# Kernel tuning notes

Measured on AMD Instinct MI355X. Metric: run time of the kernel, lower is better.

## Reference

```python
import jax, jax.numpy as jnp
import numpy as np


def setup_inputs() -> dict:
    key = jax.random.key(0)
    ks = jax.random.split(key, 4)
    B, C, H, W = 4, 512, 64, 64
    A = 512  # attention_dim
    x = jax.random.normal(ks[0], (B, C, H, W), dtype=jnp.float32)
    # 1x1 conv weights as [out_ch, in_ch] matrices (kaiming-like scale)
    scale = np.sqrt(2.0 / C).astype(np.float32)
    Wq = jax.random.normal(ks[1], (A, C), dtype=jnp.float32) * scale
    Wk = jax.random.normal(ks[2], (A, C), dtype=jnp.float32) * scale
    Wv = jax.random.normal(ks[3], (C, C), dtype=jnp.float32) * scale
    bq = jnp.zeros((A,), dtype=jnp.float32)
    bk = jnp.zeros((A,), dtype=jnp.float32)
    bv = jnp.zeros((C,), dtype=jnp.float32)
    return {"x": x, "Wq": Wq, "bq": bq, "Wk": Wk, "bk": bk, "Wv": Wv, "bv": bv}


def reference(x, Wq, bq, Wk, bk, Wv, bv):
    B, C, H, W = x.shape
    N = H * W
    xf = x.reshape(B, C, N)  # [B, C, N]
    # 1x1 convs == per-pixel channel matmuls
    q = jnp.einsum('ac,bcn->bna', Wq, xf) + bq[None, None, :]   # [B, N, A] (query, permuted)
    k = jnp.einsum('ac,bcn->ban', Wk, xf) + bk[None, :, None]   # [B, A, N] (key)
    v = jnp.einsum('oc,bcn->bno', Wv, xf) + bv[None, None, :]   # [B, N, C] (value, permuted)
    attn = jnp.einsum('bna,bam->bnm', q, k)                     # [B, N, N]
    attn = jax.nn.softmax(attn, axis=-2)                        # softmax over dim=-2 (queries)
    out = jnp.einsum('bnm,bmc->bnc', attn, v)                   # [B, N, C]
    # Faithful to torch: .view(B, C, H, W) reinterprets the [B, N, C] buffer
    out = out.reshape(B, C, H, W)
    return x + 0.1 * out
```

## Files before the change

kernel.cpp:

```cpp
#include <hip/hip_runtime.h>
#include <stdint.h>


#define LDT 40
#define SUB 5120

typedef _Float16 f16x8 __attribute__((ext_vector_type(8)));
typedef float f32x4 __attribute__((ext_vector_type(4)));

template <int ASRC, int EPI>
__global__ void __launch_bounds__(256, 2) gemm_f16(
    const _Float16* __restrict__ Ap, long lda, long zsa,
    const _Float16* __restrict__ Bp, long ldb, long zsb,
    int kslice,
    const _Float16* __restrict__ fs16, long zsl,
    float* __restrict__ outF, _Float16* __restrict__ outH, long ldc, long zso,
    const float* __restrict__ bias0, const float* __restrict__ bias1,
    const float* __restrict__ xadd,
    float* __restrict__ pmax, float* __restrict__ psum, long zsp,
    float alpha)
{
  __shared__ _Float16 smem[4 * SUB];
  _Float16* sA0 = smem;
  _Float16* sA1 = smem + SUB;
  _Float16* sB0 = smem + 2 * SUB;
  _Float16* sB1 = smem + 3 * SUB;

  const int z = blockIdx.z;
  const long i0 = (long)blockIdx.x * 128;
  const long j0 = (long)blockIdx.y * 128;
  const int t = (int)threadIdx.x;
  const int lane = t & 63;
  const int wv = t >> 6;
  const int quad = lane >> 4;
  const int lrow = lane & 15;
  const int wm = (wv & 1) << 6;
  const int wn = (wv >> 1) << 6;

  const int r0 = t >> 2;
  const int s0 = (t & 3) << 3;

  const _Float16* gA0 = Ap + z * zsa + (i0 + r0) * lda + s0;
  const _Float16* gA1 = gA0 + 64 * lda;
  const _Float16* gB0 = Bp + z * zsb + (j0 + r0) * ldb + s0;
  const _Float16* gB1 = gB0 + 64 * ldb;
  const int la0 = r0 * LDT + s0;
  const int la1 = (r0 + 64) * LDT + s0;

  const _Float16* fsZ = nullptr;
  if constexpr (ASRC == 1)
    fsZ = fs16 + z * zsl + (long)blockIdx.x * 4096 + s0;

  f32x4 acc[4][4];
  const f32x4 fz = {0.f, 0.f, 0.f, 0.f};
#pragma unroll
  for (int a = 0; a < 4; a++)
#pragma unroll
    for (int b = 0; b < 4; b++) acc[a][b] = fz;

  for (int kk = 0; kk < kslice; kk += 64) {
    f16x8 va0 = *(const f16x8*)(gA0 + kk);
    f16x8 va1 = *(const f16x8*)(gA1 + kk);
    f16x8 va2 = *(const f16x8*)(gA0 + kk + 32);
    f16x8 va3 = *(const f16x8*)(gA1 + kk + 32);
    f16x8 vb0 = *(const f16x8*)(gB0 + kk);
    f16x8 vb1 = *(const f16x8*)(gB1 + kk);
    f16x8 vb2 = *(const f16x8*)(gB0 + kk + 32);
    f16x8 vb3 = *(const f16x8*)(gB1 + kk + 32);
    if constexpr (ASRC == 1) {
      const f16x8 fsv0 = *(const f16x8*)(fsZ + kk);
      const f16x8 fsv1 = *(const f16x8*)(fsZ + kk + 32);
      va0 = va0 * fsv0;
      va1 = va1 * fsv0;
      va2 = va2 * fsv1;
      va3 = va3 * fsv1;
    }
    __syncthreads();
    *(f16x8*)&sA0[la0] = va0;
    *(f16x8*)&sA0[la1] = va1;
    *(f16x8*)&sA1[la0] = va2;
    *(f16x8*)&sA1[la1] = va3;
    *(f16x8*)&sB0[la0] = vb0;
    *(f16x8*)&sB0[la1] = vb1;
    *(f16x8*)&sB1[la0] = vb2;
    *(f16x8*)&sB1[la1] = vb3;
    __syncthreads();

#pragma unroll
    for (int h = 0; h < 2; h++) {
      const _Float16* pA = h ? sA1 : sA0;
      const _Float16* pB = h ? sB1 : sB0;
      f16x8 fa[4], fb[4];
#pragma unroll
      for (int f = 0; f < 4; f++) {
        fa[f] = *(const f16x8*)&pA[(wm + f * 16 + lrow) * LDT + quad * 8];
        fb[f] = *(const f16x8*)&pB[(wn + f * 16 + lrow) * LDT + quad * 8];
      }
#pragma unroll
      for (int fm = 0; fm < 4; fm++)
#pragma unroll
        for (int fn = 0; fn < 4; fn++)
          acc[fm][fn] = __builtin_amdgcn_mfma_f32_16x16x32_f16(fa[fm], fb[fn], acc[fm][fn], 0, 0, 0);
    }
  }

  const long obase = (long)z * zso;

  if constexpr (EPI == 1 || EPI == 2) {
#pragma unroll
    for (int fm = 0; fm < 4; fm++) {
      const long gi0 = i0 + wm + fm * 16 + quad * 4;
#pragma unroll
      for (int fn = 0; fn < 4; fn++) {
        const long gj = j0 + wn + fn * 16 + lrow;
        float badd = 0.f;
        if constexpr (EPI == 1) badd = (gj < 512) ? bias0[gj] : bias1[gj - 512];
#pragma unroll
        for (int r = 0; r < 4; r++) {
          float v = acc[fm][fn][r];
          if constexpr (EPI == 1) v += badd;
          else v += bias0[gi0 + r];
          outH[obase + (gi0 + r) * ldc + gj] = (_Float16)v;
        }
      }
    }
  } else if constexpr (EPI == 3) {
#pragma unroll
    for (int fm = 0; fm < 4; fm++) {
      const long gi0 = i0 + wm + fm * 16 + quad * 4;
#pragma unroll
      for (int fn = 0; fn < 4; fn++) {
        const long gj = j0 + wn + fn * 16 + lrow;
#pragma unroll
        for (int r = 0; r < 4; r++) {
          const long o = obase + (gi0 + r) * ldc + gj;
          outF[o] = fmaf(alpha, acc[fm][fn][r], xadd[o]);
        }
      }
    }
  } else {
    __syncthreads();
    float* Ls = (float*)smem;
#pragma unroll
    for (int fn = 0; fn < 4; fn++) {
      float mx = -3.4e38f;
#pragma unroll
      for (int fm = 0; fm < 4; fm++)
#pragma unroll
        for (int r = 0; r < 4; r++) mx = fmaxf(mx, acc[fm][fn][r]);
      float sm = 0.f;
#pragma unroll
      for (int fm = 0; fm < 4; fm++)
#pragma unroll
        for (int r = 0; r < 4; r++) sm += __expf(acc[fm][fn][r] - mx);
      Ls[(wv * 4 + quad) * 64 + fn * 16 + lrow] = mx;
      Ls[1024 + (wv * 4 + quad) * 64 + fn * 16 + lrow] = sm;
    }
    __syncthreads();
    {
      const int c = t & 127;
      const int h = t >> 7;
      const int wvv = ((c >> 6) << 1) + h;
      const int wc = c & 63;
      float M = -3.4e38f, Ss = 0.f;
#pragma unroll
      for (int q = 0; q < 4; q++) {
        float m2 = Ls[(wvv * 4 + q) * 64 + wc];
        float s2 = Ls[1024 + (wvv * 4 + q) * 64 + wc];
        float nm = fmaxf(M, m2);
        Ss = Ss * __expf(M - nm) + s2 * __expf(m2 - nm);
        M = nm;
      }
      Ls[2048 + h * 128 + c] = M;
      Ls[2304 + h * 128 + c] = Ss;
    }
    __syncthreads();
    if (t < 128) {
      float m0 = Ls[2048 + t], m1 = Ls[2048 + 128 + t];
      float sa = Ls[2304 + t], sb = Ls[2304 + 128 + t];
      float nm = fmaxf(m0, m1);
      float s = sa * __expf(m0 - nm) + sb * __expf(m1 - nm);
      const long pidx = z * zsp + (long)blockIdx.x * 4096 + j0 + t;
      pmax[pidx] = nm;
      psum[pidx] = s;
      Ls[t] = nm;
    }
    __syncthreads();
#pragma unroll
    for (int fn = 0; fn < 4; fn++) {
      const int colc = wn + fn * 16 + lrow;
      const float Mcol = Ls[colc];
      const long gj = j0 + colc;
#pragma unroll
      for (int fm = 0; fm < 4; fm++) {
        const long gi0 = i0 + wm + fm * 16 + quad * 4;
#pragma unroll
        for (int r = 0; r < 4; r++)
          outH[obase + (gi0 + r) * ldc + gj] = (_Float16)__expf(acc[fm][fn][r] - Mcol);
      }
    }
  }
}

__global__ void convert_weights(const float* __restrict__ Wq, const float* __restrict__ Wk,
                                const float* __restrict__ Wv,
                                _Float16* __restrict__ WQK, _Float16* __restrict__ Wv16)
{
  int idx = blockIdx.x * 256 + threadIdx.x;
  if (idx < 524288)
    WQK[idx] = (_Float16)((idx < 262144) ? Wq[idx] : Wk[idx - 262144]);
  else
    Wv16[idx - 524288] = (_Float16)Wv[idx - 524288];
}

__global__ void transpose_x(const float* __restrict__ x, _Float16* __restrict__ xT)
{
  __shared__ float tile[32][33];
  const int b = blockIdx.z;
  const int n0 = blockIdx.x * 32;
  const int c0 = blockIdx.y * 32;
  const int tx = threadIdx.x;
  const int ty = threadIdx.y;
  const float* xb = x + (long)b * 2097152;
#pragma unroll
  for (int k = 0; k < 4; k++)
    tile[ty + k * 8][tx] = xb[(long)(c0 + ty + k * 8) * 4096 + n0 + tx];
  __syncthreads();
  _Float16* xTb = xT + (long)b * 2097152;
#pragma unroll
  for (int k = 0; k < 4; k++)
    xTb[(long)(n0 + ty + k * 8) * 512 + c0 + tx] = (_Float16)tile[tx][ty + k * 8];
}

__global__ void stats_final(const float* __restrict__ pmax, const float* __restrict__ psum,
                            float* __restrict__ lse)
{
  const int idx = blockIdx.x * 256 + threadIdx.x;
  const int z = idx >> 12;
  const int m = idx & 4095;
  const float* pm = pmax + (long)z * 131072 + m;
  const float* ps = psum + (long)z * 131072 + m;
  float M = -3.4e38f, S = 0.f;
  for (int i = 0; i < 32; i++) {
    float m2 = pm[(long)i * 4096], s2 = ps[(long)i * 4096];
    float nm = fmaxf(M, m2);
    S = S * __expf(M - nm) + s2 * __expf(m2 - nm);
    M = nm;
  }
  lse[idx] = M + __logf(S);
}

__global__ void scale_factors(const float* __restrict__ pmax, const float* __restrict__ lse,
                              _Float16* __restrict__ fs16)
{
  const int idx = blockIdx.x * 256 + threadIdx.x;
  const int z = idx >> 17;
  const int m = idx & 4095;
  fs16[idx] = (_Float16)__expf(pmax[idx] - lse[(z << 12) + m]);
}

extern "C" void kernel_launch(void* const* d_in, const int* in_sizes, int n_in,
                              void* d_out, int out_size, void* d_ws, size_t ws_size,
                              hipStream_t stream)
{
  const float* x  = (const float*)d_in[0];
  const float* Wq = (const float*)d_in[1];
  const float* bq = (const float*)d_in[2];
  const float* Wk = (const float*)d_in[3];
  const float* bk = (const float*)d_in[4];
  const float* Wv = (const float*)d_in[5];
  const float* bv = (const float*)d_in[6];
  float* out = (float*)d_out;

  char* w = (char*)d_ws;
  _Float16* WQK   = (_Float16*)(w + 0);
  _Float16* Wv16  = (_Float16*)(w + 1048576);
  _Float16* xT    = (_Float16*)(w + 1572864);
  _Float16* QK    = (_Float16*)(w + 18350080);
  _Float16* Vt    = (_Float16*)(w + 51904512);
  float*    lse   = (float*)   (w + 68681728);
  float*    pmaxB = (float*)   (w + 68747264);
  float*    psumB = (float*)   (w + 70844416);
  _Float16* fs16  = (_Float16*)(w + 72941568);
  _Float16* S16   = (_Float16*)(w + 75038720);

  convert_weights<<<3072, 256, 0, stream>>>(Wq, Wk, Wv, WQK, Wv16);
  transpose_x<<<dim3(128, 16, 4), dim3(32, 8), 0, stream>>>(x, xT);

  gemm_f16<0, 1><<<dim3(32, 8, 4), 256, 0, stream>>>(
      xT, 512, 2097152L, WQK, 512, 0L, 512, nullptr, 0L,
      nullptr, QK, 1024, 4194304L, bq, bk, nullptr, nullptr, nullptr, 0L, 0.f);
  gemm_f16<0, 2><<<dim3(4, 32, 4), 256, 0, stream>>>(
      Wv16, 512, 0L, xT, 512, 2097152L, 512, nullptr, 0L,
      nullptr, Vt, 4096, 2097152L, bv, nullptr, nullptr, nullptr, nullptr, 0L, 0.f);
  gemm_f16<0, 4><<<dim3(32, 32, 4), 256, 0, stream>>>(
      QK, 1024, 4194304L, QK + 512, 1024, 4194304L, 512, nullptr, 0L,
      nullptr, S16, 4096, 16777216L, nullptr, nullptr, nullptr,
      pmaxB, psumB, 131072L, 0.f);
  stats_final<<<64, 256, 0, stream>>>(pmaxB, psumB, lse);
  scale_factors<<<2048, 256, 0, stream>>>(pmaxB, lse, fs16);
  gemm_f16<1, 3><<<dim3(32, 4, 4), 256, 0, stream>>>(
      S16, 4096, 16777216L, Vt, 4096, 2097152L, 4096, fs16, 131072L,
      out, nullptr, 512, 2097152L, nullptr, nullptr, x, nullptr, nullptr, 0L, 0.1f);
}
```

Measured before the change: 314.0 us.

## Parametrize GEMM k-step depth, fuse softmax stats kernels, compute column sums post-max

The GEMM template gains an NSUB parameter, so each main-loop iteration stages NSUB 32-wide k-slices per barrier pair. The final S·V GEMM uses 4 slices (128 k per iteration), which halves its barrier count at the cost of doubled shared memory. The score GEMM epilogue now finds the block column max first and then computes exp once, reusing it for both the fp16 output and the partial sums. This removes the duplicated exponentials and the online rescaling. The separate lse and scale-factor kernels are merged into one kernel with 64 blocks, which saves a launch and an intermediate buffer but gives that stage less parallelism.

```diff
diff --git a/kernel.cpp b/kernel.cpp
--- a/kernel.cpp
+++ b/kernel.cpp
@@ -8,7 +8,7 @@
 typedef _Float16 f16x8 __attribute__((ext_vector_type(8)));
 typedef float f32x4 __attribute__((ext_vector_type(4)));
 
-template <int ASRC, int EPI>
+template <int ASRC, int EPI, int NSUB>
 __global__ void __launch_bounds__(256, 2) gemm_f16(
     const _Float16* __restrict__ Ap, long lda, long zsa,
     const _Float16* __restrict__ Bp, long ldb, long zsb,
@@ -20,11 +20,7 @@
     float* __restrict__ pmax, float* __restrict__ psum, long zsp,
     float alpha)
 {
-  __shared__ _Float16 smem[4 * SUB];
-  _Float16* sA0 = smem;
-  _Float16* sA1 = smem + SUB;
-  _Float16* sB0 = smem + 2 * SUB;
-  _Float16* sB1 = smem + 3 * SUB;
+  __shared__ _Float16 smem[2 * NSUB * SUB];
 
   const int z = blockIdx.z;
   const long i0 = (long)blockIdx.x * 128;
@@ -58,38 +54,37 @@
 #pragma unroll
     for (int b = 0; b < 4; b++) acc[a][b] = fz;
 
-  for (int kk = 0; kk < kslice; kk += 64) {
-    f16x8 va0 = *(const f16x8*)(gA0 + kk);
-    f16x8 va1 = *(const f16x8*)(gA1 + kk);
-    f16x8 va2 = *(const f16x8*)(gA0 + kk + 32);
-    f16x8 va3 = *(const f16x8*)(gA1 + kk + 32);
-    f16x8 vb0 = *(const f16x8*)(gB0 + kk);
-    f16x8 vb1 = *(const f16x8*)(gB1 + kk);
-    f16x8 vb2 = *(const f16x8*)(gB0 + kk + 32);
-    f16x8 vb3 = *(const f16x8*)(gB1 + kk + 32);
+  for (int kk = 0; kk < kslice; kk += 32 * NSUB) {
+    f16x8 va[NSUB][2], vb[NSUB][2];
+#pragma unroll
+    for (int s = 0; s < NSUB; s++) {
+      va[s][0] = *(const f16x8*)(gA0 + kk + 32 * s);
+      va[s][1] = *(const f16x8*)(gA1 + kk + 32 * s);
+      vb[s][0] = *(const f16x8*)(gB0 + kk + 32 * s);
+      vb[s][1] = *(const f16x8*)(gB1 + kk + 32 * s);
+    }
     if constexpr (ASRC == 1) {
-      const f16x8 fsv0 = *(const f16x8*)(fsZ + kk);
-      const f16x8 fsv1 = *(const f16x8*)(fsZ + kk + 32);
-      va0 = va0 * fsv0;
-      va1 = va1 * fsv0;
-      va2 = va2 * fsv1;
-      va3 = va3 * fsv1;
-    }
-    __syncthreads();
-    *(f16x8*)&sA0[la0] = va0;
-    *(f16x8*)&sA0[la1] = va1;
-    *(f16x8*)&sA1[la0] = va2;
-    *(f16x8*)&sA1[la1] = va3;
-    *(f16x8*)&sB0[la0] = vb0;
-    *(f16x8*)&sB0[la1] = vb1;
-    *(f16x8*)&sB1[la0] = vb2;
-    *(f16x8*)&sB1[la1] = vb3;
-    __syncthreads();
-
-#pragma unroll
-    for (int h = 0; h < 2; h++) {
-      const _Float16* pA = h ? sA1 : sA0;
-      const _Float16* pB = h ? sB1 : sB0;
+#pragma unroll
+      for (int s = 0; s < NSUB; s++) {
+        const f16x8 fsv = *(const f16x8*)(fsZ + kk + 32 * s);
+        va[s][0] = va[s][0] * fsv;
+        va[s][1] = va[s][1] * fsv;
+      }
+    }
+    __syncthreads();
+#pragma unroll
+    for (int s = 0; s < NSUB; s++) {
+      *(f16x8*)&smem[s * SUB + la0] = va[s][0];
+      *(f16x8*)&smem[s * SUB + la1] = va[s][1];
+      *(f16x8*)&smem[(NSUB + s) * SUB + la0] = vb[s][0];
+      *(f16x8*)&smem[(NSUB + s) * SUB + la1] = vb[s][1];
+    }
+    __syncthreads();
+
+#pragma unroll
+    for (int h = 0; h < NSUB; h++) {
+      const _Float16* pA = smem + h * SUB;
+      const _Float16* pB = smem + (NSUB + h) * SUB;
       f16x8 fa[4], fb[4];
 #pragma unroll
       for (int f = 0; f < 4; f++) {
@@ -148,13 +143,7 @@
       for (int fm = 0; fm < 4; fm++)
 #pragma unroll
         for (int r = 0; r < 4; r++) mx = fmaxf(mx, acc[fm][fn][r]);
-      float sm = 0.f;
-#pragma unroll
-      for (int fm = 0; fm < 4; fm++)
-#pragma unroll
-        for (int r = 0; r < 4; r++) sm += __expf(acc[fm][fn][r] - mx);
       Ls[(wv * 4 + quad) * 64 + fn * 16 + lrow] = mx;
-      Ls[1024 + (wv * 4 + quad) * 64 + fn * 16 + lrow] = sm;
     }
     __syncthreads();
     {
@@ -162,42 +151,48 @@
       const int h = t >> 7;
       const int wvv = ((c >> 6) << 1) + h;
       const int wc = c & 63;
-      float M = -3.4e38f, Ss = 0.f;
-#pragma unroll
-      for (int q = 0; q < 4; q++) {
-        float m2 = Ls[(wvv * 4 + q) * 64 + wc];
-        float s2 = Ls[1024 + (wvv * 4 + q) * 64 + wc];
-        float nm = fmaxf(M, m2);
-        Ss = Ss * __expf(M - nm) + s2 * __expf(m2 - nm);
-        M = nm;
-      }
-      Ls[2048 + h * 128 + c] = M;
-      Ls[2304 + h * 128 + c] = Ss;
+      float M = -3.4e38f;
+#pragma unroll
+      for (int q = 0; q < 4; q++) M = fmaxf(M, Ls[(wvv * 4 + q) * 64 + wc]);
+      Ls[1024 + h * 128 + c] = M;
     }
     __syncthreads();
     if (t < 128) {
-      float m0 = Ls[2048 + t], m1 = Ls[2048 + 128 + t];
-      float sa = Ls[2304 + t], sb = Ls[2304 + 128 + t];
-      float nm = fmaxf(m0, m1);
-      float s = sa * __expf(m0 - nm) + sb * __expf(m1 - nm);
-      const long pidx = z * zsp + (long)blockIdx.x * 4096 + j0 + t;
-      pmax[pidx] = nm;
-      psum[pidx] = s;
-      Ls[t] = nm;
+      float Mcol = fmaxf(Ls[1024 + t], Ls[1152 + t]);
+      pmax[z * zsp + (long)blockIdx.x * 4096 + j0 + t] = Mcol;
+      Ls[1280 + t] = Mcol;
     }
     __syncthreads();
 #pragma unroll
     for (int fn = 0; fn < 4; fn++) {
       const int colc = wn + fn * 16 + lrow;
-      const float Mcol = Ls[colc];
+      const float Mcol = Ls[1280 + colc];
       const long gj = j0 + colc;
+      float sm = 0.f;
 #pragma unroll
       for (int fm = 0; fm < 4; fm++) {
         const long gi0 = i0 + wm + fm * 16 + quad * 4;
 #pragma unroll
-        for (int r = 0; r < 4; r++)
-          outH[obase + (gi0 + r) * ldc + gj] = (_Float16)__expf(acc[fm][fn][r] - Mcol);
-      }
+        for (int r = 0; r < 4; r++) {
+          float e = __expf(acc[fm][fn][r] - Mcol);
+          sm += e;
+          outH[obase + (gi0 + r) * ldc + gj] = (_Float16)e;
+        }
+      }
+      Ls[(wv * 4 + quad) * 64 + fn * 16 + lrow] = sm;
+    }
+    __syncthreads();
+    if (t < 128) {
+      const int wc = t & 63;
+      const int ch = t >> 6;
+      float s = 0.f;
+#pragma unroll
+      for (int h = 0; h < 2; h++) {
+        const int wvv = (ch << 1) + h;
+#pragma unroll
+        for (int q = 0; q < 4; q++) s += Ls[(wvv * 4 + q) * 64 + wc];
+      }
+      psum[z * zsp + (long)blockIdx.x * 4096 + j0 + t] = s;
     }
   }
 }
@@ -232,8 +227,8 @@
     xTb[(long)(n0 + ty + k * 8) * 512 + c0 + tx] = (_Float16)tile[tx][ty + k * 8];
 }
 
-__global__ void stats_final(const float* __restrict__ pmax, const float* __restrict__ psum,
-                            float* __restrict__ lse)
+__global__ void stats_scale(const float* __restrict__ pmax, const float* __restrict__ psum,
+                            _Float16* __restrict__ fs16)
 {
   const int idx = blockIdx.x * 256 + threadIdx.x;
   const int z = idx >> 12;
@@ -247,16 +242,10 @@
     S = S * __expf(M - nm) + s2 * __expf(m2 - nm);
     M = nm;
   }
-  lse[idx] = M + __logf(S);
-}
-
-__global__ void scale_factors(const float* __restrict__ pmax, const float* __restrict__ lse,
-                              _Float16* __restrict__ fs16)
-{
-  const int idx = blockIdx.x * 256 + threadIdx.x;
-  const int z = idx >> 17;
-  const int m = idx & 4095;
-  fs16[idx] = (_Float16)__expf(pmax[idx] - lse[(z << 12) + m]);
+  const float lse = M + __logf(S);
+  _Float16* fo = fs16 + (long)z * 131072 + m;
+  for (int i = 0; i < 32; i++)
+    fo[(long)i * 4096] = (_Float16)__expf(pm[(long)i * 4096] - lse);
 }
 
 extern "C" void kernel_launch(void* const* d_in, const int* in_sizes, int n_in,
@@ -278,7 +267,6 @@
   _Float16* xT    = (_Float16*)(w + 1572864);
   _Float16* QK    = (_Float16*)(w + 18350080);
   _Float16* Vt    = (_Float16*)(w + 51904512);
-  float*    lse   = (float*)   (w + 68681728);
   float*    pmaxB = (float*)   (w + 68747264);
   float*    psumB = (float*)   (w + 70844416);
   _Float16* fs16  = (_Float16*)(w + 72941568);
@@ -287,19 +275,18 @@
   convert_weights<<<3072, 256, 0, stream>>>(Wq, Wk, Wv, WQK, Wv16);
   transpose_x<<<dim3(128, 16, 4), dim3(32, 8), 0, stream>>>(x, xT);
 
-  gemm_f16<0, 1><<<dim3(32, 8, 4), 256, 0, stream>>>(
+  gemm_f16<0, 1, 2><<<dim3(32, 8, 4), 256, 0, stream>>>(
       xT, 512, 2097152L, WQK, 512, 0L, 512, nullptr, 0L,
       nullptr, QK, 1024, 4194304L, bq, bk, nullptr, nullptr, nullptr, 0L, 0.f);
-  gemm_f16<0, 2><<<dim3(4, 32, 4), 256, 0, stream>>>(
+  gemm_f16<0, 2, 2><<<dim3(4, 32, 4), 256, 0, stream>>>(
       Wv16, 512, 0L, xT, 512, 2097152L, 512, nullptr, 0L,
       nullptr, Vt, 4096, 2097152L, bv, nullptr, nullptr, nullptr, nullptr, 0L, 0.f);
-  gemm_f16<0, 4><<<dim3(32, 32, 4), 256, 0, stream>>>(
+  gemm_f16<0, 4, 2><<<dim3(32, 32, 4), 256, 0, stream>>>(
       QK, 1024, 4194304L, QK + 512, 1024, 4194304L, 512, nullptr, 0L,
       nullptr, S16, 4096, 16777216L, nullptr, nullptr, nullptr,
       pmaxB, psumB, 131072L, 0.f);
-  stats_final<<<64, 256, 0, stream>>>(pmaxB, psumB, lse);
-  scale_factors<<<2048, 256, 0, stream>>>(pmaxB, lse, fs16);
-  gemm_f16<1, 3><<<dim3(32, 4, 4), 256, 0, stream>>>(
+  stats_scale<<<64, 256, 0, stream>>>(pmaxB, psumB, fs16);
+  gemm_f16<1, 3, 4><<<dim3(32, 4, 4), 256, 0, stream>>>(
       S16, 4096, 16777216L, Vt, 4096, 2097152L, 4096, fs16, 131072L,
       out, nullptr, 512, 2097152L, nullptr, nullptr, x, nullptr, nullptr, 0L, 0.1f);
 }
```

Measured after the change: 311.4 us. Within noise of the previous version (-0.8%).
